# Kernel optimization log

Measured on AMD Instinct MI355X. Metric: run time of the kernel, lower is better.

The kernel has to match this reference:

```python
import jax, jax.numpy as jnp
import numpy as np

B, T, IN_DIM, D, H, F, L = 16, 64, 128, 512, 8, 2048, 4  # T == DATA_ROUNDS_PER_GAME
HD = D // H
SCALE = 1.0 / np.sqrt(HD)
NEG = -1e9


def setup_inputs() -> dict:
    key = jax.random.key(0)
    ks = jax.random.split(key, 10)
    s = lambda k, shape, fan: (jax.random.normal(k, shape, jnp.float32) * (fan ** -0.5)).astype(jnp.float32)
    return {
        "x": jax.random.normal(ks[0], (B, T, IN_DIM), jnp.float32),
        "fc_w": s(ks[1], (IN_DIM, D), IN_DIM), "fc_b": jnp.zeros((D,), jnp.float32),
        "w_qkv": s(ks[2], (L, D, 3 * D), D), "b_qkv": jnp.zeros((L, 3 * D), jnp.float32),
        "w_o": s(ks[3], (L, D, D), D), "b_o": jnp.zeros((L, D), jnp.float32),
        "ln1_g": jnp.ones((L, D), jnp.float32), "ln1_b": jnp.zeros((L, D), jnp.float32),
        "w_ff1": s(ks[4], (L, D, F), D), "b_ff1": jnp.zeros((L, F), jnp.float32),
        "w_ff2": s(ks[5], (L, F, D), F), "b_ff2": jnp.zeros((L, D), jnp.float32),
        "ln2_g": jnp.ones((L, D), jnp.float32), "ln2_b": jnp.zeros((L, D), jnp.float32),
        "cls_w1": s(ks[6], (D, D // 2), D), "cls_b1": jnp.zeros((D // 2,), jnp.float32),
        "cls_w2": s(ks[7], (D // 2, 2), D // 2), "cls_b2": jnp.zeros((2,), jnp.float32),
    }


def _ln(x, g, b, eps=1e-5):
    m = x.mean(-1, keepdims=True)
    v = ((x - m) ** 2).mean(-1, keepdims=True)
    return (x - m) * jax.lax.rsqrt(v + eps) * g + b


def _encoder(h, bias, w_qkv, b_qkv, w_o, b_o, ln1_g, ln1_b, w_ff1, b_ff1, w_ff2, b_ff2, ln2_g, ln2_b):
    # post-norm TransformerEncoderLayer (PyTorch default), dropout=0
    for l in range(L):
        Bh, Th = h.shape[0], h.shape[1]
        qkv = h @ w_qkv[l] + b_qkv[l]                      # [B,T,3D]
        q, k, v = jnp.split(qkv, 3, axis=-1)
        q = q.reshape(Bh, Th, H, HD)
        k = k.reshape(Bh, Th, H, HD)
        v = v.reshape(Bh, Th, H, HD)
        scores = jnp.einsum('bqhd,bkhd->bhqk', q, k) * SCALE + bias
        attn = jax.nn.softmax(scores, axis=-1)
        o = jnp.einsum('bhqk,bkhd->bqhd', attn, v).reshape(Bh, Th, D)
        h = _ln(h + o @ w_o[l] + b_o[l], ln1_g[l], ln1_b[l])
        ff = jax.nn.relu(h @ w_ff1[l] + b_ff1[l]) @ w_ff2[l] + b_ff2[l]
        h = _ln(h + ff, ln2_g[l], ln2_b[l])
    return h


def reference(x, fc_w, fc_b, w_qkv, b_qkv, w_o, b_o, ln1_g, ln1_b, w_ff1, b_ff1,
              w_ff2, b_ff2, ln2_g, ln2_b, cls_w1, cls_b1, cls_w2, cls_b2):
    h0 = jax.nn.relu(x @ fc_w + fc_b)                       # [B,T,D]

    def per_prefix(i):
        # keys restricted to positions <= i reproduces re-running the encoder
        # on the prefix x[:, :i+1]; we read position i (the prefix's last token).
        keep = jnp.arange(T) <= i
        bias = jnp.where(keep, 0.0, NEG).astype(h0.dtype)[None, None, None, :]  # [1,1,1,T]
        out = _encoder(h0, bias, w_qkv, b_qkv, w_o, b_o, ln1_g, ln1_b,
                       w_ff1, b_ff1, w_ff2, b_ff2, ln2_g, ln2_b)
        return jnp.take(out, i, axis=1)                     # [B,D]

    y = jax.vmap(per_prefix)(jnp.arange(T))                 # [T,B,D]
    y = jnp.transpose(y, (1, 0, 2))                         # [B,T,D]
    z = jax.nn.relu(y @ cls_w1 + cls_b1) @ cls_w2 + cls_b2  # [B,T,2]
    return jax.nn.log_softmax(z, axis=-1)
```

## Files before the change

### kernel.cpp

```cpp
#include <hip/hip_runtime.h>
#include <math.h>

using u16 = unsigned short;
using u32 = unsigned int;

constexpr int Bc = 16;
constexpr int Tc = 64;
constexpr int INc = 128;
constexpr int Dc = 512;
constexpr int Hc = 8;
constexpr int Fc = 2048;
constexpr int Lc = 4;
constexpr float SCALEc = 0.125f;

constexpr int NGc = 3;
constexpr int g_p0[NGc]   = {0, 35, 51};
constexpr int g_np[NGc]   = {35, 16, 13};
constexpr int g_start[NGc]= {0, 12160, 24192};
constexpr int g_M[NGc]    = {12288, 12032, 12672};
constexpr int g_M3[NGc]   = {640, 256, 256};
constexpr int g_doff[NGc] = {0, 560, 816};
constexpr int GMAXc = 12672;
constexpr int DALLc = 1024;
constexpr int DPADc = 1152;
constexpr int VTSc  = GMAXc + 64;

typedef __attribute__((ext_vector_type(8))) short bf16x8;
typedef __attribute__((ext_vector_type(4))) float f32x4;

__device__ __forceinline__ int rowbase(int p) {
  const int q = p >> 3, r = p & 7;
  return 128 * (4 * q * (q + 1) + r * (q + 1));
}

__device__ __forceinline__ float bf2f(u16 u) {
  union { u32 i; float f; } c; c.i = (u32)u << 16; return c.f;
}
__device__ __forceinline__ u16 f2bf(float f) {
  union { float f; u32 u; } c{f};
  u32 r = (c.u + 0x7fffu + ((c.u >> 16) & 1u)) >> 16;
  return (u16)r;
}

template<bool RELU>
__global__ __launch_bounds__(256) void gemm_kernel(
    const float* __restrict__ A, const float* __restrict__ W,
    const float* __restrict__ bias, float* __restrict__ C,
    u16* __restrict__ Cb, int M, int K, int N)
{
  __shared__ float As[128][17];
  __shared__ float Ws[16][64];
  const int tid = threadIdx.x;
  const int tx = tid & 15, ty = tid >> 4;
  const int row0 = blockIdx.y * 128, col0 = blockIdx.x * 64;
  float acc[8][4];
#pragma unroll
  for (int i = 0; i < 8; ++i)
#pragma unroll
    for (int j = 0; j < 4; ++j) acc[i][j] = 0.f;
  const int ar = tid >> 1, ak = (tid & 1) * 8;
  const int wr = tid >> 4, wc = (tid & 15) * 4;
  for (int k0 = 0; k0 < K; k0 += 16) {
    const float* ap = A + (size_t)(row0 + ar) * K + k0 + ak;
    float4 a0 = *(const float4*)ap;
    float4 a1 = *(const float4*)(ap + 4);
    As[ar][ak+0]=a0.x; As[ar][ak+1]=a0.y; As[ar][ak+2]=a0.z; As[ar][ak+3]=a0.w;
    As[ar][ak+4]=a1.x; As[ar][ak+5]=a1.y; As[ar][ak+6]=a1.z; As[ar][ak+7]=a1.w;
    *(float4*)&Ws[wr][wc] = *(const float4*)(W + (size_t)(k0 + wr) * N + col0 + wc);
    __syncthreads();
#pragma unroll
    for (int kk = 0; kk < 16; ++kk) {
      const float4 w4 = *(const float4*)&Ws[kk][tx * 4];
#pragma unroll
      for (int i = 0; i < 8; ++i) {
        const float av = As[ty + 16 * i][kk];
        acc[i][0] += av * w4.x; acc[i][1] += av * w4.y;
        acc[i][2] += av * w4.z; acc[i][3] += av * w4.w;
      }
    }
    __syncthreads();
  }
#pragma unroll
  for (int i = 0; i < 8; ++i) {
    const int r = row0 + ty + 16 * i, c = col0 + tx * 4;
    float4 v;
    v.x = acc[i][0] + bias[c+0]; v.y = acc[i][1] + bias[c+1];
    v.z = acc[i][2] + bias[c+2]; v.w = acc[i][3] + bias[c+3];
    if (RELU) { v.x=fmaxf(v.x,0.f); v.y=fmaxf(v.y,0.f); v.z=fmaxf(v.z,0.f); v.w=fmaxf(v.w,0.f); }
    *(float4*)&C[(size_t)r * N + c] = v;
    uint2 pk;
    pk.x = (u32)f2bf(v.x) | ((u32)f2bf(v.y) << 16);
    pk.y = (u32)f2bf(v.z) | ((u32)f2bf(v.w) << 16);
    *(uint2*)&Cb[(size_t)r * N + c] = pk;
  }
}

__global__ __launch_bounds__(256) void transpose_conv(
    const float* __restrict__ src, u16* __restrict__ dst, int K, int N)
{
  __shared__ float t[32][33];
  const int bx = blockIdx.x * 32;
  const int by = blockIdx.y * 32;
  const int x = threadIdx.x, y = threadIdx.y;
#pragma unroll
  for (int i = 0; i < 32; i += 8) t[y + i][x] = src[(size_t)(by + y + i) * N + bx + x];
  __syncthreads();
#pragma unroll
  for (int i = 0; i < 32; i += 8)
    dst[(size_t)(bx + y + i) * K + by + x] = f2bf(t[x][y + i]);
}

__global__ __launch_bounds__(256) void transpose_v(
    const u16* __restrict__ qkvsrc, u16* __restrict__ vt, int vstride)
{
  __shared__ u16 t[64][65];
  const int r0 = blockIdx.x * 64;
  const int d0 = blockIdx.y * 64;
  const int tid = threadIdx.x;
  const int rr = tid >> 2, cc = (tid & 3) * 16;
  const u16* src = qkvsrc + (size_t)(r0 + rr) * 1536 + 1024 + d0 + cc;
  union { uint4 v; u16 s[8]; } ua, ub;
  ua.v = *(const uint4*)src;
  ub.v = *(const uint4*)(src + 8);
#pragma unroll
  for (int i = 0; i < 8; ++i) { t[rr][cc + i] = ua.s[i]; t[rr][cc + 8 + i] = ub.s[i]; }
  __syncthreads();
  const int dd = tid >> 2, kk = (tid & 3) * 16;
  union { uint4 v; u16 s[8]; } w0, w1;
#pragma unroll
  for (int i = 0; i < 8; ++i) { w0.s[i] = t[kk + i][dd]; w1.s[i] = t[kk + 8 + i][dd]; }
  u16* dst = vt + (size_t)(d0 + dd) * vstride + r0 + kk;
  *(uint4*)dst = w0.v;
  *(uint4*)(dst + 8) = w1.v;
}

__device__ __forceinline__ void stage_tile(const u16* __restrict__ src, int ldk, u16* lds)
{
  const int tid = threadIdx.x;
#pragma unroll
  for (int q = 0; q < 4; ++q) {
    const int p16 = tid + (q << 8);
    const int row = p16 >> 3;
    const int s   = p16 & 7;
    const int k16 = s ^ (row & 7);
    const u16* g = src + (size_t)row * ldk + (k16 << 3);
    __builtin_amdgcn_global_load_lds(
        (const __attribute__((address_space(1))) void*)g,
        (__attribute__((address_space(3))) void*)(lds + (p16 << 3)),
        16, 0, 0);
  }
}

template<bool RELU, bool OUT_BF16>
__global__ __launch_bounds__(256) void gemm_mfma(
    const u16* __restrict__ A, const u16* __restrict__ Wt,
    const float* __restrict__ bias, void* __restrict__ Cout,
    int M, int K, int N)
{
  __shared__ u16 As[2][128 * 64];
  __shared__ u16 Bs[2][128 * 64];

  const int tid  = threadIdx.x;
  const int lane = tid & 63;
  const int wave = tid >> 6;
  const int wr = wave >> 1;
  const int wc = wave & 1;

  const int gx = gridDim.x;
  const int nwg = gx * gridDim.y;
  const int lin = blockIdx.y * gx + blockIdx.x;
  const int qq = nwg >> 3, r8 = nwg & 7;
  const int xcd = lin & 7, pos = lin >> 3;
  const int orig = (xcd < r8) ? (xcd * (qq + 1) + pos)
                              : (r8 * (qq + 1) + (xcd - r8) * qq + pos);
  const int row0 = (orig / gx) * 128;
  const int col0 = (orig % gx) * 128;

  f32x4 acc[4][4];
#pragma unroll
  for (int i = 0; i < 4; ++i)
#pragma unroll
    for (int j = 0; j < 4; ++j) acc[i][j] = f32x4{0.f, 0.f, 0.f, 0.f};

  const int nk = K >> 6;
  const int arow = wr * 64 + (lane & 15);
  const int brow = wc * 64 + (lane & 15);
  const int kq   = lane >> 4;

  stage_tile(A  + (size_t)row0 * K, K, &As[0][0]);
  stage_tile(Wt + (size_t)col0 * K, K, &Bs[0][0]);

  for (int t = 0; t < nk; ++t) {
    const int cur = t & 1;
    if (t + 1 < nk) {
      const int k0 = (t + 1) << 6;
      stage_tile(A  + (size_t)row0 * K + k0, K, &As[cur ^ 1][0]);
      stage_tile(Wt + (size_t)col0 * K + k0, K, &Bs[cur ^ 1][0]);
      asm volatile("s_waitcnt vmcnt(8)\n\ts_barrier" ::: "memory");
    } else {
      asm volatile("s_waitcnt vmcnt(0)\n\ts_barrier" ::: "memory");
    }
    const u16* Ab = &As[cur][0];
    const u16* Bb = &Bs[cur][0];
#pragma unroll
    for (int kk = 0; kk < 2; ++kk) {
      bf16x8 af[4], bfr[4];
      const int c = kk * 4 + kq;
#pragma unroll
      for (int i = 0; i < 4; ++i) {
        const int ra = arow + i * 16;
        af[i]  = *reinterpret_cast<const bf16x8*>(Ab + ra * 64 + ((c ^ (ra & 7)) << 3));
        const int rb = brow + i * 16;
        bfr[i] = *reinterpret_cast<const bf16x8*>(Bb + rb * 64 + ((c ^ (rb & 7)) << 3));
      }
#pragma unroll
      for (int mi = 0; mi < 4; ++mi)
#pragma unroll
        for (int ni = 0; ni < 4; ++ni)
          acc[mi][ni] = __builtin_amdgcn_mfma_f32_16x16x32_bf16(af[mi], bfr[ni], acc[mi][ni], 0, 0, 0);
    }
    asm volatile("s_barrier" ::: "memory");
  }

  const int r0 = row0 + wr * 64 + ((lane >> 4) << 2);
  const int c0 = col0 + wc * 64 + (lane & 15);
#pragma unroll
  for (int mi = 0; mi < 4; ++mi)
#pragma unroll
    for (int ni = 0; ni < 4; ++ni) {
      const int col = c0 + ni * 16;
      const float bsv = bias[col];
#pragma unroll
      for (int j = 0; j < 4; ++j) {
        const int row = r0 + mi * 16 + j;
        float o = acc[mi][ni][j] + bsv;
        if (RELU) o = fmaxf(o, 0.f);
        if (OUT_BF16) ((u16*)Cout)[(size_t)row * N + col] = f2bf(o);
        else          ((float*)Cout)[(size_t)row * N + col] = o;
      }
    }
}

template<bool SHARED>
__global__ __launch_bounds__(64) void attn_mfma_kernel(
    const u16* __restrict__ qkv, const u16* __restrict__ vt, int vstride,
    u16* __restrict__ attno, int p0, int gstart)
{
  const int hh = blockIdx.x, b = blockIdx.y, p = p0 + blockIdx.z;
  const int NT = p + 1;
  const int NT8 = (NT + 7) & ~7;
  const int rb = rowbase(p) + b * NT8 - gstart;
  const int sb = SHARED ? (b * 64) : rb;
  const int tid = threadIdx.x;
  const int lc = tid & 15, lg = tid >> 4;

  __shared__ u16 Plds[64][72];
  __shared__ u16 VTl[4096];
  __shared__ float invl[64];

  {
    const u16* vbase = vt + (size_t)(hh * 64) * vstride + sb;
#pragma unroll
    for (int it = 0; it < 8; ++it) {
      const int gi = tid + (it << 6);
      const int dd = gi >> 3, s = gi & 7;
      const u16* src = vbase + (size_t)dd * vstride + ((s ^ (dd & 7)) << 3);
      __builtin_amdgcn_global_load_lds(
          (const __attribute__((address_space(1))) void*)src,
          (__attribute__((address_space(3))) void*)(&VTl[gi << 3]), 16, 0, 0);
    }
  }

  f32x4 st[4][4];
#pragma unroll
  for (int i = 0; i < 4; ++i)
#pragma unroll
    for (int j = 0; j < 4; ++j) st[i][j] = f32x4{0.f, 0.f, 0.f, 0.f};

#pragma unroll
  for (int kt = 0; kt < 2; ++kt) {
    bf16x8 kf[4], qf[4];
#pragma unroll
    for (int t = 0; t < 4; ++t) {
      if (t * 16 < NT) {
        const size_t rbase = (size_t)(sb + t * 16 + lc) * 1536 + hh * 64 + kt * 32 + lg * 8;
        qf[t] = *reinterpret_cast<const bf16x8*>(qkv + rbase);
        kf[t] = *reinterpret_cast<const bf16x8*>(qkv + rbase + 512);
      }
    }
#pragma unroll
    for (int mi = 0; mi < 4; ++mi)
      if (mi * 16 < NT)
#pragma unroll
        for (int ni = 0; ni < 4; ++ni)
          if (ni * 16 < NT)
            st[mi][ni] = __builtin_amdgcn_mfma_f32_16x16x32_bf16(kf[mi], qf[ni], st[mi][ni], 0, 0, 0);
  }

#pragma unroll
  for (int ni = 0; ni < 4; ++ni) {
    float mm = -3.0e38f;
#pragma unroll
    for (int mi = 0; mi < 4; ++mi)
#pragma unroll
      for (int e = 0; e < 4; ++e)
        if (16 * mi + 4 * lg + e < NT) mm = fmaxf(mm, st[mi][ni][e]);
    mm = fmaxf(mm, __shfl_xor(mm, 16));
    mm = fmaxf(mm, __shfl_xor(mm, 32));
    float ss = 0.f;
#pragma unroll
    for (int mi = 0; mi < 4; ++mi) {
      u16 pb[4];
#pragma unroll
      for (int e = 0; e < 4; ++e) {
        const float pe = (16 * mi + 4 * lg + e < NT)
                           ? __expf((st[mi][ni][e] - mm) * SCALEc) : 0.f;
        ss += pe;
        pb[e] = f2bf(pe);
      }
      uint2 pk;
      pk.x = (u32)pb[0] | ((u32)pb[1] << 16);
      pk.y = (u32)pb[2] | ((u32)pb[3] << 16);
      *reinterpret_cast<uint2*>(&Plds[16 * ni + lc][16 * mi + 4 * lg]) = pk;
    }
    ss += __shfl_xor(ss, 16);
    ss += __shfl_xor(ss, 32);
    if (lg == 0) invl[16 * ni + lc] = 1.f / ss;
  }

  asm volatile("s_waitcnt vmcnt(0)" ::: "memory");
  __syncthreads();

  f32x4 oc[4][4];
#pragma unroll
  for (int i = 0; i < 4; ++i)
#pragma unroll
    for (int j = 0; j < 4; ++j) oc[i][j] = f32x4{0.f, 0.f, 0.f, 0.f};

#pragma unroll
  for (int kt = 0; kt < 2; ++kt) {
    if (kt * 32 < NT) {
      bf16x8 pa[4], vbf[4];
#pragma unroll
      for (int t = 0; t < 4; ++t) {
        if (t * 16 < NT)
          pa[t] = *reinterpret_cast<const bf16x8*>(&Plds[t * 16 + lc][kt * 32 + lg * 8]);
        const int dd = t * 16 + lc;
        vbf[t] = *reinterpret_cast<const bf16x8*>(
            &VTl[dd * 64 + (((4 * kt + lg) ^ (lc & 7)) << 3)]);
      }
#pragma unroll
      for (int qt = 0; qt < 4; ++qt)
        if (qt * 16 < NT)
#pragma unroll
          for (int dt = 0; dt < 4; ++dt)
            oc[qt][dt] = __builtin_amdgcn_mfma_f32_16x16x32_bf16(pa[qt], vbf[dt], oc[qt][dt], 0, 0, 0);
    }
  }

#pragma unroll
  for (int qt = 0; qt < 4; ++qt) {
    if (qt * 16 < NT) {
#pragma unroll
      for (int e = 0; e < 4; ++e) {
        const int qrow = qt * 16 + 4 * lg + e;
        if (qrow < NT) {
          const float inv = invl[qrow];
          u16* dst = attno + (size_t)(rb + qrow) * Dc + hh * 64 + lc;
#pragma unroll
          for (int dt = 0; dt < 4; ++dt)
            dst[dt * 16] = f2bf(oc[qt][dt][e] * inv);
        }
      }
    }
  }
}

__global__ __launch_bounds__(64) void attn_diag_kernel(
    const u16* __restrict__ kv3, const u16* __restrict__ qd,
    u16* __restrict__ attno_d, int p0, int gstart, int doff)
{
  const int hh = blockIdx.x, b = blockIdx.y, pl = blockIdx.z;
  const int p = p0 + pl;
  const int NT = p + 1;
  const int NT8 = (NT + 7) & ~7;
  const int rb = rowbase(p) + b * NT8 - gstart;
  const int tid = threadIdx.x;
  const int rd = doff + pl * 16 + b;

  __shared__ u16 Ks[64][64];
  __shared__ u16 Vs[64][64];

  const int lrow = tid >> 3;
  const int lc8  = tid & 7;
  for (int t0 = 0; t0 < NT; t0 += 8) {
    const int tr = rb + t0 + lrow;
    const int csrc = (lc8 ^ lrow) << 3;
    const u16* gk = kv3 + (size_t)tr * 1024 + hh * 64 + csrc;
    const u16* gv = kv3 + (size_t)tr * 1024 + 512 + hh * 64 + csrc;
    __builtin_amdgcn_global_load_lds(
        (const __attribute__((address_space(1))) void*)gk,
        (__attribute__((address_space(3))) void*)(&Ks[t0][0] + tid * 8), 16, 0, 0);
    __builtin_amdgcn_global_load_lds(
        (const __attribute__((address_space(1))) void*)gv,
        (__attribute__((address_space(3))) void*)(&Vs[t0][0] + tid * 8), 16, 0, 0);
  }

  const u16* qp = qd + (size_t)rd * Dc + hh * 64;
  float qv[64];
#pragma unroll
  for (int c8 = 0; c8 < 8; ++c8) {
    const bf16x8 q8 = *reinterpret_cast<const bf16x8*>(qp + c8 * 8);
#pragma unroll
    for (int i = 0; i < 8; ++i) qv[c8 * 8 + i] = bf2f((u16)q8[i]);
  }
  asm volatile("s_waitcnt vmcnt(0)" ::: "memory");
  __syncthreads();

  float dot = -1e30f;
  if (tid < NT) {
    dot = 0.f;
#pragma unroll
    for (int c8 = 0; c8 < 8; ++c8) {
      const bf16x8 k8 = *reinterpret_cast<const bf16x8*>(
          &Ks[tid][0] + ((c8 ^ (tid & 7)) << 3));
#pragma unroll
      for (int i = 0; i < 8; ++i) dot += qv[c8 * 8 + i] * bf2f((u16)k8[i]);
    }
    dot *= SCALEc;
  }
  float mm = dot;
#pragma unroll
  for (int off = 32; off; off >>= 1) mm = fmaxf(mm, __shfl_xor(mm, off));
  const float pt = __expf(dot - mm);
  float s = pt;
#pragma unroll
  for (int off = 32; off; off >>= 1) s += __shfl_xor(s, off);
  const float inv = 1.f / s;

  float o = 0.f;
  for (int t = 0; t < NT; ++t) {
    const float ptt = __shfl(pt, t);
    o += ptt * bf2f(Vs[t][(((tid >> 3) ^ (t & 7)) << 3) + (tid & 7)]);
  }
  attno_d[(size_t)rd * Dc + hh * 64 + tid] = f2bf(o * inv);
}

__device__ inline float wave_sum(float v) {
#pragma unroll
  for (int off = 32; off; off >>= 1) v += __shfl_xor(v, off);
  return v;
}

__global__ __launch_bounds__(256) void res_ln_kernel(
    float* __restrict__ h, u16* __restrict__ hb, const u16* __restrict__ tmpb,
    const float* __restrict__ g, const float* __restrict__ bt)
{
  const size_t row = (size_t)blockIdx.x * 4 + (threadIdx.x >> 6);
  const int t = threadIdx.x & 63;
  float v[8];
  float s = 0.f;
#pragma unroll
  for (int i = 0; i < 8; ++i) {
    v[i] = h[row * Dc + i * 64 + t] + bf2f(tmpb[row * Dc + i * 64 + t]);
    s += v[i];
  }
  s = wave_sum(s);
  const float mean = s * (1.f / 512.f);
  float vs = 0.f;
#pragma unroll
  for (int i = 0; i < 8; ++i) { const float d = v[i] - mean; vs += d * d; }
  vs = wave_sum(vs);
  const float rstd = rsqrtf(vs * (1.f / 512.f) + 1e-5f);
#pragma unroll
  for (int i = 0; i < 8; ++i) {
    const float o = (v[i] - mean) * rstd * g[i * 64 + t] + bt[i * 64 + t];
    h[row * Dc + i * 64 + t] = o;
    hb[row * Dc + i * 64 + t] = f2bf(o);
  }
}

__global__ __launch_bounds__(64) void res_ln0_kernel(
    const float* __restrict__ h0, float* __restrict__ h, u16* __restrict__ hb,
    const u16* __restrict__ tmpb, const float* __restrict__ g,
    const float* __restrict__ bt, int p0, int gstart)
{
  const int t = blockIdx.x, b = blockIdx.y, p = p0 + blockIdx.z;
  if (t > p) return;
  const int NT8 = (p + 8) & ~7;
  const size_t row = (size_t)(rowbase(p) + b * NT8 + t - gstart);
  const int tt = threadIdx.x;
  const float* src = h0 + (size_t)(b * 64 + t) * Dc;
  float v[8];
  float s = 0.f;
#pragma unroll
  for (int i = 0; i < 8; ++i) {
    v[i] = src[i * 64 + tt] + bf2f(tmpb[row * Dc + i * 64 + tt]);
    s += v[i];
  }
  s = wave_sum(s);
  const float mean = s * (1.f / 512.f);
  float vs = 0.f;
#pragma unroll
  for (int i = 0; i < 8; ++i) { const float d = v[i] - mean; vs += d * d; }
  vs = wave_sum(vs);
  const float rstd = rsqrtf(vs * (1.f / 512.f) + 1e-5f);
#pragma unroll
  for (int i = 0; i < 8; ++i) {
    const float o = (v[i] - mean) * rstd * g[i * 64 + tt] + bt[i * 64 + tt];
    h[row * Dc + i * 64 + tt] = o;
    hb[row * Dc + i * 64 + tt] = f2bf(o);
  }
}

__global__ __launch_bounds__(128) void gather_diag(
    const float* __restrict__ h, float* __restrict__ hd, u16* __restrict__ hbd,
    int p0, int gstart, int doff)
{
  const int pl = blockIdx.x >> 4, b = blockIdx.x & 15;
  const int p = p0 + pl;
  const int NT8 = (p + 8) & ~7;
  const size_t src = (size_t)(rowbase(p) + b * NT8 + p - gstart);
  const size_t rd = doff + blockIdx.x;
  const float4 v = ((const float4*)(h + src * Dc))[threadIdx.x];
  ((float4*)(hd + rd * Dc))[threadIdx.x] = v;
  uint2 pk;
  pk.x = (u32)f2bf(v.x) | ((u32)f2bf(v.y) << 16);
  pk.y = (u32)f2bf(v.z) | ((u32)f2bf(v.w) << 16);
  ((uint2*)(hbd + rd * Dc))[threadIdx.x] = pk;
}

__global__ __launch_bounds__(128) void scatter_out(
    const float* __restrict__ hd, float* __restrict__ yb, int p0, int doff)
{
  const int pl = blockIdx.x >> 4, b = blockIdx.x & 15;
  const int p = p0 + pl;
  ((float4*)(yb + ((size_t)(b * 64 + p)) * Dc))[threadIdx.x] =
      ((const float4*)(hd + (size_t)(doff + blockIdx.x) * Dc))[threadIdx.x];
}

__global__ __launch_bounds__(256) void cls_kernel(
    const float* __restrict__ y, const float* __restrict__ w1, const float* __restrict__ b1,
    const float* __restrict__ w2, const float* __restrict__ b2, float* __restrict__ out)
{
  const int row = blockIdx.x;
  const int j = threadIdx.x;
  __shared__ float ys[512];
  ys[j]       = y[(size_t)row * Dc + j];
  ys[j + 256] = y[(size_t)row * Dc + 256 + j];
  __syncthreads();

  float acc = b1[j];
  for (int d = 0; d < 512; ++d) acc += ys[d] * w1[(size_t)d * 256 + j];
  acc = fmaxf(acc, 0.f);

  float c0 = acc * w2[j * 2 + 0];
  float c1 = acc * w2[j * 2 + 1];
  c0 = wave_sum(c0);
  c1 = wave_sum(c1);

  __shared__ float r0[4], r1[4];
  const int w = j >> 6, lane = j & 63;
  if (lane == 0) { r0[w] = c0; r1[w] = c1; }
  __syncthreads();
  if (j == 0) {
    const float z0 = r0[0] + r0[1] + r0[2] + r0[3] + b2[0];
    const float z1 = r1[0] + r1[1] + r1[2] + r1[3] + b2[1];
    const float mz = fmaxf(z0, z1);
    const float lse = mz + logf(expf(z0 - mz) + expf(z1 - mz));
    out[row * 2 + 0] = z0 - lse;
    out[row * 2 + 1] = z1 - lse;
  }
}

extern "C" void kernel_launch(void* const* d_in, const int* in_sizes, int n_in,
                              void* d_out, int out_size, void* d_ws, size_t ws_size,
                              hipStream_t stream)
{
  if (n_in < 19) return;
  const float* x      = (const float*)d_in[0];
  const float* fc_w   = (const float*)d_in[1];
  const float* fc_b   = (const float*)d_in[2];
  const float* w_qkv  = (const float*)d_in[3];
  const float* b_qkv  = (const float*)d_in[4];
  const float* w_o    = (const float*)d_in[5];
  const float* b_o    = (const float*)d_in[6];
  const float* ln1_g  = (const float*)d_in[7];
  const float* ln1_b  = (const float*)d_in[8];
  const float* w_ff1  = (const float*)d_in[9];
  const float* b_ff1  = (const float*)d_in[10];
  const float* w_ff2  = (const float*)d_in[11];
  const float* b_ff2  = (const float*)d_in[12];
  const float* ln2_g  = (const float*)d_in[13];
  const float* ln2_b  = (const float*)d_in[14];
  const float* cls_w1 = (const float*)d_in[15];
  const float* cls_b1 = (const float*)d_in[16];
  const float* cls_w2 = (const float*)d_in[17];
  const float* cls_b2 = (const float*)d_in[18];
  float* out = (float*)d_out;

  char* wp = (char*)d_ws;
  auto alloc = [&](size_t bytes) -> char* {
    char* p = wp; wp += (bytes + 255) & ~(size_t)255; return p;
  };
  float* h0  = (float*)alloc((size_t)Bc * Tc * Dc * 4);
  u16*   h0b = (u16*)  alloc((size_t)Bc * Tc * Dc * 2);
  float* yb  = (float*)alloc((size_t)Bc * Tc * Dc * 4);
  u16*   qkv0= (u16*)  alloc((size_t)Bc * Tc * 3 * Dc * 2);
  u16*   vt0 = (u16*)  alloc((size_t)Dc * Bc * Tc * 2);
  u16 *wtq[Lc], *wto[Lc], *wtf1[Lc], *wtf2[Lc];
  for (int l = 0; l < Lc; ++l) {
    wtq[l]  = (u16*)alloc((size_t)3 * Dc * Dc * 2);
    wto[l]  = (u16*)alloc((size_t)Dc * Dc * 2);
    wtf1[l] = (u16*)alloc((size_t)Fc * Dc * 2);
    wtf2[l] = (u16*)alloc((size_t)Dc * Fc * 2);
  }
  const size_t RS = (size_t)GMAXc + 64;
  float* h     = (float*)alloc((size_t)GMAXc * Dc * 4);
  u16*   hb    = (u16*)  alloc((size_t)GMAXc * Dc * 2);
  u16*   qkvb  = (u16*)  alloc(RS * 3 * Dc * 2);
  u16*   attno = (u16*)  alloc((size_t)GMAXc * Dc * 2);
  u16*   tmpb  = (u16*)  alloc((size_t)GMAXc * Dc * 2);
  u16*   ffb   = (u16*)  alloc((size_t)GMAXc * Fc * 2);
  u16*   vt    = (u16*)  alloc((size_t)Dc * VTSc * 2);
  float* hdiag = (float*)alloc((size_t)DPADc * Dc * 4);
  u16*   hbdiag= (u16*)  alloc((size_t)DPADc * Dc * 2);
  u16*   attnd = (u16*)  alloc((size_t)DPADc * Dc * 2);
  u16*   qd    = (u16*)  alloc((size_t)DPADc * Dc * 2);
  if ((size_t)(wp - (char*)d_ws) > ws_size) return;
  u16* kv3 = qkvb;

  const dim3 tb(32, 8);
  for (int l = 0; l < Lc; ++l) {
    transpose_conv<<<dim3(3 * Dc / 32, Dc / 32), tb, 0, stream>>>(
        w_qkv + (size_t)l * Dc * 3 * Dc, wtq[l], Dc, 3 * Dc);
    transpose_conv<<<dim3(Dc / 32, Dc / 32), tb, 0, stream>>>(
        w_o + (size_t)l * Dc * Dc, wto[l], Dc, Dc);
    transpose_conv<<<dim3(Fc / 32, Dc / 32), tb, 0, stream>>>(
        w_ff1 + (size_t)l * Dc * Fc, wtf1[l], Dc, Fc);
    transpose_conv<<<dim3(Dc / 32, Fc / 32), tb, 0, stream>>>(
        w_ff2 + (size_t)l * Fc * Dc, wtf2[l], Fc, Dc);
  }

  gemm_kernel<true><<<dim3(Dc / 64, (Bc * Tc) / 128), 256, 0, stream>>>(
      x, fc_w, fc_b, h0, h0b, Bc * Tc, INc, Dc);

  gemm_mfma<false, true><<<dim3(3 * Dc / 128, (Bc * Tc) / 128), 256, 0, stream>>>(
      h0b, wtq[0], b_qkv, qkv0, Bc * Tc, Dc, 3 * Dc);
  transpose_v<<<dim3((Bc * Tc) / 64, 8), 256, 0, stream>>>(qkv0, vt0, Bc * Tc);

  for (int g = 0; g < NGc; ++g) {
    const int p0 = g_p0[g], np = g_np[g], gs = g_start[g], Mg = g_M[g];
    const int M3 = g_M3[g], doff = g_doff[g];

    attn_mfma_kernel<true><<<dim3(Hc, Bc, np), 64, 0, stream>>>(
        qkv0, vt0, Bc * Tc, attno, p0, gs);
    gemm_mfma<false, true><<<dim3(Dc / 128, Mg / 128), 256, 0, stream>>>(
        attno, wto[0], b_o, tmpb, Mg, Dc, Dc);
    res_ln0_kernel<<<dim3(64, 16, np), 64, 0, stream>>>(
        h0, h, hb, tmpb, ln1_g, ln1_b, p0, gs);
    gemm_mfma<true, true><<<dim3(Fc / 128, Mg / 128), 256, 0, stream>>>(
        hb, wtf1[0], b_ff1, ffb, Mg, Dc, Fc);
    gemm_mfma<false, true><<<dim3(Dc / 128, Mg / 128), 256, 0, stream>>>(
        ffb, wtf2[0], b_ff2, tmpb, Mg, Fc, Dc);
    res_ln_kernel<<<Mg / 4, 256, 0, stream>>>(h, hb, tmpb, ln2_g, ln2_b);

    for (int l = 1; l < 3; ++l) {
      gemm_mfma<false, true><<<dim3(3 * Dc / 128, Mg / 128), 256, 0, stream>>>(
          hb, wtq[l], b_qkv + (size_t)l * 3 * Dc, qkvb, Mg, Dc, 3 * Dc);
      transpose_v<<<dim3(Mg / 64, 8), 256, 0, stream>>>(qkvb, vt, VTSc);
      attn_mfma_kernel<false><<<dim3(Hc, Bc, np), 64, 0, stream>>>(
          qkvb, vt, VTSc, attno, p0, gs);
      gemm_mfma<false, true><<<dim3(Dc / 128, Mg / 128), 256, 0, stream>>>(
          attno, wto[l], b_o + (size_t)l * Dc, tmpb, Mg, Dc, Dc);
      res_ln_kernel<<<Mg / 4, 256, 0, stream>>>(h, hb, tmpb, ln1_g + l * Dc, ln1_b + l * Dc);
      gemm_mfma<true, true><<<dim3(Fc / 128, Mg / 128), 256, 0, stream>>>(
          hb, wtf1[l], b_ff1 + (size_t)l * Fc, ffb, Mg, Dc, Fc);
      gemm_mfma<false, true><<<dim3(Dc / 128, Mg / 128), 256, 0, stream>>>(
          ffb, wtf2[l], b_ff2 + (size_t)l * Dc, tmpb, Mg, Fc, Dc);
      res_ln_kernel<<<Mg / 4, 256, 0, stream>>>(h, hb, tmpb, ln2_g + l * Dc, ln2_b + l * Dc);
    }

    {
      const int l = 3;
      gather_diag<<<np * 16, 128, 0, stream>>>(h, hdiag, hbdiag, p0, gs, doff);
      gemm_mfma<false, true><<<dim3(Dc / 128, M3 / 128), 256, 0, stream>>>(
          hbdiag + (size_t)doff * Dc, wtq[l], b_qkv + (size_t)l * 3 * Dc,
          qd + (size_t)doff * Dc, M3, Dc, Dc);
      gemm_mfma<false, true><<<dim3(2 * Dc / 128, Mg / 128), 256, 0, stream>>>(
          hb, wtq[l] + (size_t)512 * Dc, b_qkv + (size_t)l * 3 * Dc + 512,
          kv3, Mg, Dc, 2 * Dc);
      attn_diag_kernel<<<dim3(Hc, Bc, np), 64, 0, stream>>>(
          kv3, qd, attnd, p0, gs, doff);
    }
  }

  {
    const int l = 3;
    gemm_mfma<false, true><<<dim3(Dc / 128, DALLc / 128), 256, 0, stream>>>(
        attnd, wto[l], b_o + (size_t)l * Dc, tmpb, DALLc, Dc, Dc);
    res_ln_kernel<<<DALLc / 4, 256, 0, stream>>>(hdiag, hbdiag, tmpb,
                                                 ln1_g + l * Dc, ln1_b + l * Dc);
    gemm_mfma<true, true><<<dim3(Fc / 128, DALLc / 128), 256, 0, stream>>>(
        hbdiag, wtf1[l], b_ff1 + (size_t)l * Fc, ffb, DALLc, Dc, Fc);
    gemm_mfma<false, true><<<dim3(Dc / 128, DALLc / 128), 256, 0, stream>>>(
        ffb, wtf2[l], b_ff2 + (size_t)l * Dc, tmpb, DALLc, Fc, Dc);
    res_ln_kernel<<<DALLc / 4, 256, 0, stream>>>(hdiag, hbdiag, tmpb,
                                                 ln2_g + l * Dc, ln2_b + l * Dc);
    for (int g = 0; g < NGc; ++g)
      scatter_out<<<g_np[g] * 16, 128, 0, stream>>>(hdiag, yb, g_p0[g], g_doff[g]);
  }

  cls_kernel<<<Bc * Tc, 256, 0, stream>>>(yb, cls_w1, cls_b1, cls_w2, cls_b2, out);
}
```

Baseline: 1.687 ms.

## Add 256x256-tile MFMA GEMM with async LDS loads for FF1 and QKV

Adds a new GEMM kernel with 256x256 output tiles and 512 threads. It stages A and B into swizzled LDS through global_load_lds, uses a multi-slot pipeline with explicit vmcnt waits, remaps blocks across XCDs, and raises wave priority around the MFMA bursts. The FF1 and layer 1-2 QKV GEMMs now use it, so M is padded up to a multiple of 256 and the group-3 buffer sizes grow to match. The aim is more data reuse per tile and fewer LDS and global loads per FLOP. The costs are more padded rows of work and heavy register and LDS pressure.

```diff
diff --git a/kernel.cpp b/kernel.cpp
--- a/kernel.cpp
+++ b/kernel.cpp
@@ -18,12 +18,13 @@
 constexpr int g_np[NGc]   = {35, 16, 13};
 constexpr int g_start[NGc]= {0, 12160, 24192};
 constexpr int g_M[NGc]    = {12288, 12032, 12672};
-constexpr int g_M3[NGc]   = {640, 256, 256};
+constexpr int g_M2[NGc]   = {12288, 12032, 12800};
+constexpr int g_M3[NGc]   = {768, 256, 256};
 constexpr int g_doff[NGc] = {0, 560, 816};
-constexpr int GMAXc = 12672;
+constexpr int GMAXc = 12800;
 constexpr int DALLc = 1024;
 constexpr int DPADc = 1152;
-constexpr int VTSc  = GMAXc + 64;
+constexpr int VTSc  = 12672 + 64;
 
 typedef __attribute__((ext_vector_type(8))) short bf16x8;
 typedef __attribute__((ext_vector_type(4))) float f32x4;
@@ -239,6 +240,154 @@
         else          ((float*)Cout)[(size_t)row * N + col] = o;
       }
     }
+}
+
+__device__ __forceinline__ void stage_half512(const u16* __restrict__ src, int ldk, u16* lds)
+{
+  const int tid = threadIdx.x;
+#pragma unroll
+  for (int q = 0; q < 2; ++q) {
+    const int p16 = tid + (q << 9);
+    const int row = p16 >> 3;
+    const int s   = p16 & 7;
+    const int k16 = s ^ (row & 7);
+    const u16* g = src + (size_t)row * ldk + (k16 << 3);
+    __builtin_amdgcn_global_load_lds(
+        (const __attribute__((address_space(1))) void*)g,
+        (__attribute__((address_space(3))) void*)(lds + (p16 << 3)),
+        16, 0, 0);
+  }
+}
+
+#define PHASE256(SLOT, LRBASE, ACC)                                           \
+  do {                                                                        \
+    bf16x8 af[4][2];                                                          \
+    _Pragma("unroll")                                                         \
+    for (int m = 0; m < 4; ++m) {                                             \
+      const int lr = (LRBASE) + m * 16 + lc;                                  \
+      _Pragma("unroll")                                                       \
+      for (int ks = 0; ks < 2; ++ks) {                                        \
+        const int c = ks * 4 + lg;                                            \
+        af[m][ks] = *reinterpret_cast<const bf16x8*>(                         \
+            (SLOT) + lr * 64 + ((c ^ (lr & 7)) << 3));                        \
+      }                                                                       \
+    }                                                                         \
+    __builtin_amdgcn_s_setprio(1);                                            \
+    _Pragma("unroll")                                                         \
+    for (int m = 0; m < 4; ++m)                                               \
+      _Pragma("unroll")                                                       \
+      for (int n = 0; n < 2; ++n)                                             \
+        _Pragma("unroll")                                                     \
+        for (int ks = 0; ks < 2; ++ks)                                        \
+          ACC[m][n] = __builtin_amdgcn_mfma_f32_16x16x32_bf16(                \
+              af[m][ks], bfr[n][ks], ACC[m][n], 0, 0, 0);                     \
+    __builtin_amdgcn_s_setprio(0);                                            \
+  } while (0)
+
+template<bool RELU, bool OUT_BF16>
+__global__ __launch_bounds__(512, 2) void gemm_mfma256(
+    const u16* __restrict__ A, const u16* __restrict__ Wt,
+    const float* __restrict__ bias, void* __restrict__ Cout,
+    int M, int K, int N)
+{
+  __shared__ u16 As[4][128 * 64];
+  __shared__ u16 Bs[2][256 * 64];
+
+  const int tid  = threadIdx.x;
+  const int lane = tid & 63;
+  const int w    = tid >> 6;
+  const int lc = lane & 15, lg = lane >> 4;
+
+  const int gx = gridDim.x;
+  const int nwg = gx * gridDim.y;
+  const int lin = blockIdx.y * gx + blockIdx.x;
+  const int qq = nwg >> 3, r8 = nwg & 7;
+  const int xcd = lin & 7, pos = lin >> 3;
+  const int orig = (xcd < r8) ? (xcd * (qq + 1) + pos)
+                              : (r8 * (qq + 1) + (xcd - r8) * qq + pos);
+  const int row0 = (orig / gx) * 256;
+  const int col0 = (orig % gx) * 256;
+
+  f32x4 acc0[4][2], acc1[4][2], acc2[4][2], acc3[4][2];
+#pragma unroll
+  for (int m = 0; m < 4; ++m)
+#pragma unroll
+    for (int n = 0; n < 2; ++n) {
+      acc0[m][n] = f32x4{0.f,0.f,0.f,0.f}; acc1[m][n] = f32x4{0.f,0.f,0.f,0.f};
+      acc2[m][n] = f32x4{0.f,0.f,0.f,0.f}; acc3[m][n] = f32x4{0.f,0.f,0.f,0.f};
+    }
+
+  const int nk = K >> 6;
+  const u16* Abase = A  + (size_t)row0 * K;
+  const u16* Bbase = Wt + (size_t)col0 * K;
+
+  stage_half512(Abase, K, As[0]);
+  stage_half512(Bbase, K, Bs[0]);
+  stage_half512(Bbase + (size_t)128 * K, K, Bs[0] + 128 * 64);
+  stage_half512(Abase + (size_t)128 * K, K, As[1]);
+
+  for (int t = 0; t < nk; ++t) {
+    const int d  = t & 1;
+    const int s0 = (2 * t) & 3, s1 = (2 * t + 1) & 3;
+    const int sn0 = (2 * t + 2) & 3, sn1 = (2 * t + 3) & 3;
+    const bool pre = (t + 1 < nk);
+    const int k0n = (t + 1) << 6;
+
+    asm volatile("s_waitcnt vmcnt(2)\n\ts_barrier" ::: "memory");
+
+    bf16x8 bfr[2][2];
+#pragma unroll
+    for (int n = 0; n < 2; ++n) {
+      const int rb = w * 32 + n * 16 + lc;
+#pragma unroll
+      for (int ks = 0; ks < 2; ++ks) {
+        const int c = ks * 4 + lg;
+        bfr[n][ks] = *reinterpret_cast<const bf16x8*>(
+            Bs[d] + rb * 64 + ((c ^ (rb & 7)) << 3));
+      }
+    }
+
+    if (pre) {
+      stage_half512(Abase + k0n, K, As[sn0]);
+      stage_half512(Bbase + k0n, K, Bs[d ^ 1]);
+    }
+    PHASE256(As[s0], 0, acc0);
+
+    if (pre) stage_half512(Bbase + (size_t)128 * K + k0n, K, Bs[d ^ 1] + 128 * 64);
+    PHASE256(As[s0], 64, acc1);
+
+    if (pre) asm volatile("s_waitcnt vmcnt(6)\n\ts_barrier" ::: "memory");
+    else     asm volatile("s_waitcnt vmcnt(0)\n\ts_barrier" ::: "memory");
+
+    if (pre) stage_half512(Abase + (size_t)128 * K + k0n, K, As[sn1]);
+    PHASE256(As[s1], 0, acc2);
+
+    PHASE256(As[s1], 64, acc3);
+  }
+
+  const int c0 = col0 + w * 32 + lc;
+#pragma unroll
+  for (int p = 0; p < 4; ++p) {
+#pragma unroll
+    for (int m = 0; m < 4; ++m) {
+      const int rbase = row0 + p * 64 + m * 16 + lg * 4;
+#pragma unroll
+      for (int n = 0; n < 2; ++n) {
+        const int col = c0 + n * 16;
+        const float bsv = bias[col];
+        const f32x4 a = (p == 0) ? acc0[m][n] : (p == 1) ? acc1[m][n]
+                       : (p == 2) ? acc2[m][n] : acc3[m][n];
+#pragma unroll
+        for (int j = 0; j < 4; ++j) {
+          const int row = rbase + j;
+          float o = a[j] + bsv;
+          if (RELU) o = fmaxf(o, 0.f);
+          if (OUT_BF16) ((u16*)Cout)[(size_t)row * N + col] = f2bf(o);
+          else          ((float*)Cout)[(size_t)row * N + col] = o;
+        }
+      }
+    }
+  }
 }
 
 template<bool SHARED>
@@ -650,7 +799,8 @@
   transpose_v<<<dim3((Bc * Tc) / 64, 8), 256, 0, stream>>>(qkv0, vt0, Bc * Tc);
 
   for (int g = 0; g < NGc; ++g) {
-    const int p0 = g_p0[g], np = g_np[g], gs = g_start[g], Mg = g_M[g];
+    const int p0 = g_p0[g], np = g_np[g], gs = g_start[g];
+    const int Mg = g_M[g], Mg2 = g_M2[g];
     const int M3 = g_M3[g], doff = g_doff[g];
 
     attn_mfma_kernel<true><<<dim3(Hc, Bc, np), 64, 0, stream>>>(
@@ -659,23 +809,23 @@
         attno, wto[0], b_o, tmpb, Mg, Dc, Dc);
     res_ln0_kernel<<<dim3(64, 16, np), 64, 0, stream>>>(
         h0, h, hb, tmpb, ln1_g, ln1_b, p0, gs);
-    gemm_mfma<true, true><<<dim3(Fc / 128, Mg / 128), 256, 0, stream>>>(
-        hb, wtf1[0], b_ff1, ffb, Mg, Dc, Fc);
+    gemm_mfma256<true, true><<<dim3(Fc / 256, Mg2 / 256), 512, 0, stream>>>(
+        hb, wtf1[0], b_ff1, ffb, Mg2, Dc, Fc);
     gemm_mfma<false, true><<<dim3(Dc / 128, Mg / 128), 256, 0, stream>>>(
         ffb, wtf2[0], b_ff2, tmpb, Mg, Fc, Dc);
     res_ln_kernel<<<Mg / 4, 256, 0, stream>>>(h, hb, tmpb, ln2_g, ln2_b);
 
     for (int l = 1; l < 3; ++l) {
-      gemm_mfma<false, true><<<dim3(3 * Dc / 128, Mg / 128), 256, 0, stream>>>(
-          hb, wtq[l], b_qkv + (size_t)l * 3 * Dc, qkvb, Mg, Dc, 3 * Dc);
+      gemm_mfma256<false, true><<<dim3(3 * Dc / 256, Mg2 / 256), 512, 0, stream>>>(
+          hb, wtq[l], b_qkv + (size_t)l * 3 * Dc, qkvb, Mg2, Dc, 3 * Dc);
       transpose_v<<<dim3(Mg / 64, 8), 256, 0, stream>>>(qkvb, vt, VTSc);
       attn_mfma_kernel<false><<<dim3(Hc, Bc, np), 64, 0, stream>>>(
           qkvb, vt, VTSc, attno, p0, gs);
       gemm_mfma<false, true><<<dim3(Dc / 128, Mg / 128), 256, 0, stream>>>(
           attno, wto[l], b_o + (size_t)l * Dc, tmpb, Mg, Dc, Dc);
       res_ln_kernel<<<Mg / 4, 256, 0, stream>>>(h, hb, tmpb, ln1_g + l * Dc, ln1_b + l * Dc);
-      gemm_mfma<true, true><<<dim3(Fc / 128, Mg / 128), 256, 0, stream>>>(
-          hb, wtf1[l], b_ff1 + (size_t)l * Fc, ffb, Mg, Dc, Fc);
+      gemm_mfma256<true, true><<<dim3(Fc / 256, Mg2 / 256), 512, 0, stream>>>(
+          hb, wtf1[l], b_ff1 + (size_t)l * Fc, ffb, Mg2, Dc, Fc);
       gemm_mfma<false, true><<<dim3(Dc / 128, Mg / 128), 256, 0, stream>>>(
           ffb, wtf2[l], b_ff2 + (size_t)l * Dc, tmpb, Mg, Fc, Dc);
       res_ln_kernel<<<Mg / 4, 256, 0, stream>>>(h, hb, tmpb, ln2_g + l * Dc, ln2_b + l * Dc);
```

Result: slower. 1.784 ms (+5.8%).
